# Kernel tuning notes

Hardware: AMD Instinct MI355X
Metric: run time of the kernel (lower is better)

## Reference

```python
import jax, jax.numpy as jnp
import numpy as np

B, T, HID = 2, 2048, 4096
H, KV, D = 32, 4, 128
GROUP = H // KV
SCALE = D ** -0.5
EPS = 1e-6
ROPE_BASE = 10000.0


def rope(x, dims=D, base=ROPE_BASE):
    # mlx-style non-traditional RoPE (rotate halves). x: [B, h, T, D]
    t = x.shape[2]
    inv_freq = base ** (-jnp.arange(0, dims, 2, dtype=jnp.float32) / dims)  # [D/2]
    theta = jnp.arange(t, dtype=jnp.float32)[:, None] * inv_freq[None, :]   # [T, D/2]
    cos, sin = jnp.cos(theta), jnp.sin(theta)
    x1, x2 = x[..., : dims // 2], x[..., dims // 2 :]
    return jnp.concatenate([x1 * cos - x2 * sin, x1 * sin + x2 * cos], axis=-1).astype(x.dtype)


def setup_inputs() -> dict:
    key = jax.random.key(0)
    k1, k2, k3 = jax.random.split(key, 3)
    hidden_states = jax.random.normal(k1, (B, T, HID), dtype=jnp.float32)
    Wqkv = jax.random.normal(k2, ((H + 2 * KV) * D, HID), dtype=jnp.float32) * 0.02
    Wo = jax.random.normal(k3, (HID, H * D), dtype=jnp.float32) * 0.02
    q_weight = jnp.ones((H, D), dtype=jnp.float32)
    k_weight = jnp.ones((KV, D), dtype=jnp.float32)
    return {"hidden_states": hidden_states, "Wqkv": Wqkv, "Wo": Wo,
            "q_weight": q_weight, "k_weight": k_weight}


def reference(hidden_states, Wqkv, Wo, q_weight, k_weight):
    x = hidden_states
    qkv = jnp.einsum('btc,oc->bto', x, Wqkv)
    q, k, v = jnp.split(qkv, [H * D, H * D + KV * D], axis=-1)
    q = q.reshape(B, T, H, D).transpose(0, 2, 1, 3)    # [B,H,T,D]
    k = k.reshape(B, T, KV, D).transpose(0, 2, 1, 3)   # [B,KV,T,D]
    v = v.reshape(B, T, KV, D).transpose(0, 2, 1, 3)
    # Faithful to source: q/k are REPLACED by rsqrt(mean(q^2)) * weight (no q multiply)
    q = jax.lax.rsqrt(jnp.mean(q * q, axis=-1, keepdims=True) + EPS) * q_weight[:, None, :]
    k = jax.lax.rsqrt(jnp.mean(k * k, axis=-1, keepdims=True) + EPS) * k_weight[:, None, :]
    q = rope(q)
    k = rope(k)
    # GQA: repeat kv heads
    k = jnp.repeat(k, GROUP, axis=1)  # [B,H,T,D]
    v = jnp.repeat(v, GROUP, axis=1)
    scores = jnp.einsum('bhqd,bhkd->bhqk', q, k) * SCALE
    attn = jax.nn.softmax(scores, axis=-1)
    out = jnp.einsum('bhqk,bhkd->bhqd', attn, v)
    out = out.transpose(0, 2, 1, 3).reshape(B, T, H * D)
    return jnp.einsum('bto,co->btc', out, Wo)
```

## Files before the change

### kernel.cpp

```cpp
#include <hip/hip_runtime.h>

typedef __bf16 bf16_t;
typedef __bf16 bf16x4 __attribute__((ext_vector_type(4)));
typedef __bf16 bf16x8 __attribute__((ext_vector_type(8)));
typedef float floatx4 __attribute__((ext_vector_type(4)));

__device__ __forceinline__ float bf2f(bf16_t x) { return (float)x; }
__device__ __forceinline__ bf16_t f2bf(float x) { return (bf16_t)x; }

__device__ __forceinline__ void async_copy16(const bf16_t* g, bf16_t* l) {
    __builtin_amdgcn_global_load_lds(
        (const __attribute__((address_space(1))) unsigned int*)g,
        (__attribute__((address_space(3))) unsigned int*)l, 16, 0, 0);
}

__global__ __launch_bounds__(256) void cvt_f32_bf16(const float* __restrict__ in,
                                                    bf16_t* __restrict__ out,
                                                    int n8) {
    int i = blockIdx.x * blockDim.x + threadIdx.x;
    if (i >= n8) return;
    const float4* p = (const float4*)in + (size_t)i * 2;
    float4 a = p[0], b = p[1];
    bf16x8 v;
    v[0] = f2bf(a.x); v[1] = f2bf(a.y); v[2] = f2bf(a.z); v[3] = f2bf(a.w);
    v[4] = f2bf(b.x); v[5] = f2bf(b.y); v[6] = f2bf(b.z); v[7] = f2bf(b.w);
    *(bf16x8*)(out + (size_t)i * 8) = v;
}

template <typename OT>
__global__ __launch_bounds__(256) void gemm_bt(const bf16_t* __restrict__ A,
                                               const bf16_t* __restrict__ B,
                                               OT* __restrict__ C,
                                               int M, int N, int K) {
    __shared__ __attribute__((aligned(16))) bf16_t As[128 * 32];
    __shared__ __attribute__((aligned(16))) bf16_t Bs[128 * 32];
    const int tid = threadIdx.x;
    const int lane = tid & 63;
    const int w = tid >> 6;
    const int l15 = lane & 15, qd = lane >> 4;
    const int tm = blockIdx.y * 128, tn = blockIdx.x * 128;
    const int wm = (w >> 1) * 64, wn = (w & 1) * 64;

    floatx4 acc[4][4] = {};

    for (int k0 = 0; k0 < K; k0 += 32) {
#pragma unroll
        for (int it = 0; it < 2; ++it) {
            int c = it * 256 + tid;
            int row = c >> 2, col = (c & 3) * 8;
            async_copy16(&A[(size_t)(tm + row) * K + k0 + col], &As[c * 8]);
            async_copy16(&B[(size_t)(tn + row) * K + k0 + col], &Bs[c * 8]);
        }
        __syncthreads();
        bf16x8 af[4], bfr[4];
#pragma unroll
        for (int i = 0; i < 4; i++)
            af[i] = *(const bf16x8*)&As[(wm + i * 16 + l15) * 32 + qd * 8];
#pragma unroll
        for (int j = 0; j < 4; j++)
            bfr[j] = *(const bf16x8*)&Bs[(wn + j * 16 + l15) * 32 + qd * 8];
#pragma unroll
        for (int i = 0; i < 4; i++)
#pragma unroll
            for (int j = 0; j < 4; j++)
                acc[i][j] = __builtin_amdgcn_mfma_f32_16x16x32_bf16(
                    af[i], bfr[j], acc[i][j], 0, 0, 0);
        __syncthreads();
    }
#pragma unroll
    for (int i = 0; i < 4; i++) {
        int row = tm + wm + i * 16 + qd * 4;
#pragma unroll
        for (int j = 0; j < 4; j++) {
            int col = tn + wn + j * 16 + l15;
#pragma unroll
            for (int r = 0; r < 4; r++)
                C[(size_t)(row + r) * N + col] = (OT)acc[i][j][r];
        }
    }
}

__global__ __launch_bounds__(256) void rmsrope(const bf16_t* __restrict__ qkv,
                                               const float* __restrict__ qw,
                                               const float* __restrict__ kw,
                                               bf16_t* __restrict__ q_r,
                                               bf16_t* __restrict__ k_r,
                                               bf16_t* __restrict__ v_r) {
    const int tid = threadIdx.x, lane = tid & 63, w = tid >> 6;
    const int slot = blockIdx.x * 4 + w;
    const int row = slot / 40;
    const int hs = slot - row * 40;
    const int b = row >> 11, t = row & 2047;
    const bf16_t* src = qkv + (size_t)row * 5120 + hs * 128;

    if (hs >= 36) {
        size_t dst = ((size_t)((b * 4 + (hs - 36)) * 2048 + t)) * 128;
        v_r[dst + lane] = src[lane];
        v_r[dst + lane + 64] = src[lane + 64];
        return;
    }
    float x1 = bf2f(src[lane]);
    float x2 = bf2f(src[lane + 64]);
    float ss = x1 * x1 + x2 * x2;
#pragma unroll
    for (int off = 1; off < 64; off <<= 1) ss += __shfl_xor(ss, off);
    const float rr = rsqrtf(ss * (1.0f / 128.0f) + 1e-6f);

    const float* wp;
    bf16_t* dstp;
    float sc;
    if (hs < 32) {
        wp = qw + hs * 128;
        dstp = q_r + ((size_t)((b * 32 + hs) * 2048 + t)) * 128;
        sc = rr * (0.08838834764831845f * 1.4426950408889634f);
    } else {
        wp = kw + (hs - 32) * 128;
        dstp = k_r + ((size_t)((b * 4 + (hs - 32)) * 2048 + t)) * 128;
        sc = rr;
    }
    float n1 = sc * wp[lane];
    float n2 = sc * wp[lane + 64];
    float inv_freq = exp2f((float)lane * -0.20762050593046f);
    float th = (float)t * inv_freq;
    float sn, cs;
    sincosf(th, &sn, &cs);
    dstp[lane] = f2bf(n1 * cs - n2 * sn);
    dstp[lane + 64] = f2bf(n1 * sn + n2 * cs);
}

__global__ __launch_bounds__(256, 2) void flash_attn(const bf16_t* __restrict__ Qr,
                                                     const bf16_t* __restrict__ Kr,
                                                     const bf16_t* __restrict__ Vr,
                                                     bf16_t* __restrict__ Oo) {
    __shared__ __attribute__((aligned(16))) bf16_t Ks[64 * 128];
    __shared__ __attribute__((aligned(16))) bf16_t Vts[128 * 72];
    __shared__ __attribute__((aligned(16))) bf16_t Ps[4][32 * 72];
    const int tid = threadIdx.x, lane = tid & 63, w = tid >> 6;
    const int l15 = lane & 15, qd = lane >> 4;
    const int qt = blockIdx.x, bh = blockIdx.y;
    const int b = bh >> 5, h = bh & 31;
    const int kvh = h >> 3;
    const bf16_t* Qb = Qr + ((size_t)(b * 32 + h) * 2048 + qt * 128) * 128;
    const bf16_t* Kb = Kr + ((size_t)(b * 4 + kvh) * 2048) * 128;
    const bf16_t* Vb = Vr + ((size_t)(b * 4 + kvh) * 2048) * 128;
    const int wrow = w * 32;
    const int pi = l15 * 4 + qd;

    bf16x8 qf[2][4];
#pragma unroll
    for (int i = 0; i < 2; i++)
#pragma unroll
        for (int kk = 0; kk < 4; kk++)
            qf[i][kk] = *(const bf16x8*)&Qb[(size_t)(wrow + i * 16 + l15) * 128 +
                                            kk * 32 + qd * 8];

    bf16x8 onef;
#pragma unroll
    for (int e = 0; e < 8; ++e) onef[e] = f2bf(1.0f);

    float m_s[2][4];
    floatx4 lacc[2] = {};
    floatx4 oacc[2][8] = {};
#pragma unroll
    for (int i = 0; i < 2; i++)
#pragma unroll
        for (int r = 0; r < 4; r++) m_s[i][r] = -1e30f;

    for (int kt = 0; kt < 32; ++kt) {
        __syncthreads();
#pragma unroll
        for (int it = 0; it < 4; ++it) {
            int cc = it * 256 + tid;
            int row = cc >> 4;
            int xb = ((cc & 15) * 16) ^ ((row & 7) << 4);
            async_copy16(&Kb[(size_t)(kt * 64 + row) * 128 + (xb >> 1)],
                         &Ks[cc * 8]);
        }
#pragma unroll
        for (int it = 0; it < 4; ++it) {
            int d0 = (it * 4 + w) * 8;
            bf16x8 v = *(const bf16x8*)&Vb[(size_t)(kt * 64 + lane) * 128 + d0];
#pragma unroll
            for (int e = 0; e < 8; ++e) Vts[(d0 + e) * 72 + pi] = v[e];
        }
        __syncthreads();

        floatx4 sacc[2][4] = {};
#pragma unroll
        for (int kk = 0; kk < 4; kk++) {
            bf16x8 bfr[4];
#pragma unroll
            for (int j = 0; j < 4; j++) {
                int rr2 = j * 16 + l15;
                int xb = (kk * 64 + qd * 16) ^ ((rr2 & 7) << 4);
                bfr[j] = *(const bf16x8*)&Ks[rr2 * 128 + (xb >> 1)];
            }
#pragma unroll
            for (int i = 0; i < 2; i++)
#pragma unroll
                for (int j = 0; j < 4; j++)
                    sacc[i][j] = __builtin_amdgcn_mfma_f32_16x16x32_bf16(
                        qf[i][kk], bfr[j], sacc[i][j], 0, 0, 0);
        }

        float mxv[2][4];
        int fneed = 0;
#pragma unroll
        for (int i = 0; i < 2; i++)
#pragma unroll
            for (int r = 0; r < 4; r++) {
                float mx = fmaxf(fmaxf(sacc[i][0][r], sacc[i][1][r]),
                                 fmaxf(sacc[i][2][r], sacc[i][3][r]));
#pragma unroll
                for (int off = 1; off < 16; off <<= 1)
                    mx = fmaxf(mx, __shfl_xor(mx, off));
                mxv[i][r] = mx;
                fneed |= (mx > m_s[i][r] + 11.5f);
            }
        if (__any(fneed)) {
#pragma unroll
            for (int i = 0; i < 2; i++)
#pragma unroll
                for (int r = 0; r < 4; r++) {
                    float mnew = fmaxf(m_s[i][r], mxv[i][r]);
                    float alpha = exp2f(m_s[i][r] - mnew);
                    m_s[i][r] = mnew;
#pragma unroll
                    for (int jo = 0; jo < 8; jo++) oacc[i][jo][r] *= alpha;
                    lacc[i][r] *= alpha;
                }
        }
#pragma unroll
        for (int i = 0; i < 2; i++)
#pragma unroll
            for (int r = 0; r < 4; r++) {
                float m = m_s[i][r];
                bf16x4 pv;
                pv[0] = f2bf(exp2f(sacc[i][0][r] - m));
                pv[1] = f2bf(exp2f(sacc[i][1][r] - m));
                pv[2] = f2bf(exp2f(sacc[i][2][r] - m));
                pv[3] = f2bf(exp2f(sacc[i][3][r] - m));
                *(bf16x4*)&Ps[w][(i * 16 + qd * 4 + r) * 72 + l15 * 4] = pv;
            }

#pragma unroll
        for (int kk = 0; kk < 64; kk += 32) {
            bf16x8 pf[2], vf[8];
#pragma unroll
            for (int i = 0; i < 2; i++)
                pf[i] = *(const bf16x8*)&Ps[w][(i * 16 + l15) * 72 + kk + qd * 8];
#pragma unroll
            for (int jo = 0; jo < 8; jo++)
                vf[jo] = *(const bf16x8*)&Vts[(jo * 16 + l15) * 72 + kk + qd * 8];
#pragma unroll
            for (int i = 0; i < 2; i++) {
                lacc[i] = __builtin_amdgcn_mfma_f32_16x16x32_bf16(
                    pf[i], onef, lacc[i], 0, 0, 0);
#pragma unroll
                for (int jo = 0; jo < 8; jo++)
                    oacc[i][jo] = __builtin_amdgcn_mfma_f32_16x16x32_bf16(
                        pf[i], vf[jo], oacc[i][jo], 0, 0, 0);
            }
        }
    }

#pragma unroll
    for (int i = 0; i < 2; i++) {
#pragma unroll
        for (int r = 0; r < 4; r++) {
            float inv = 1.0f / lacc[i][r];
            int tg = qt * 128 + wrow + i * 16 + qd * 4 + r;
            size_t base = ((size_t)b * 2048 + tg) * 4096 + h * 128;
#pragma unroll
            for (int jo = 0; jo < 8; jo++)
                Oo[base + jo * 16 + l15] = f2bf(oacc[i][jo][r] * inv);
        }
    }
}

extern "C" void kernel_launch(void* const* d_in, const int* in_sizes, int n_in,
                              void* d_out, int out_size, void* d_ws, size_t ws_size,
                              hipStream_t stream) {
    const float* hidden = (const float*)d_in[0];
    const float* Wqkv   = (const float*)d_in[1];
    const float* Wo     = (const float*)d_in[2];
    const float* qw     = (const float*)d_in[3];
    const float* kw     = (const float*)d_in[4];
    float* out = (float*)d_out;

    char* ws = (char*)d_ws;
    bf16_t* Wqkv_bf   = (bf16_t*)ws;
    bf16_t* q_r       = (bf16_t*)ws;
    bf16_t* k_r       = (bf16_t*)(ws + 33554432ull);
    bf16_t* v_r       = (bf16_t*)(ws + 37748736ull);
    bf16_t* hidden_bf = (bf16_t*)(ws + 41943040ull);
    bf16_t* attn      = (bf16_t*)(ws + 41943040ull);
    bf16_t* qkv       = (bf16_t*)(ws + 75497472ull);
    bf16_t* Wo_bf     = (bf16_t*)(ws + 75497472ull);

    hipLaunchKernelGGL(cvt_f32_bf16, dim3(8192), dim3(256), 0, stream,
                       hidden, hidden_bf, 16777216 / 8);
    hipLaunchKernelGGL(cvt_f32_bf16, dim3(10240), dim3(256), 0, stream,
                       Wqkv, Wqkv_bf, 20971520 / 8);
    hipLaunchKernelGGL((gemm_bt<bf16_t>), dim3(40, 32), dim3(256), 0, stream,
                       hidden_bf, Wqkv_bf, qkv, 4096, 5120, 4096);
    hipLaunchKernelGGL(rmsrope, dim3(40960), dim3(256), 0, stream,
                       qkv, qw, kw, q_r, k_r, v_r);
    hipLaunchKernelGGL(cvt_f32_bf16, dim3(8192), dim3(256), 0, stream,
                       Wo, Wo_bf, 16777216 / 8);
    hipLaunchKernelGGL(flash_attn, dim3(16, 64), dim3(256), 0, stream,
                       q_r, k_r, v_r, attn);
    hipLaunchKernelGGL((gemm_bt<float>), dim3(32, 32), dim3(256), 0, stream,
                       attn, Wo_bf, out, 4096, 4096, 4096);
}
```

Baseline: 957.7 us.

## Register-prefetch next K/V tile, use DPP row max, raise attention occupancy

Replaces the async global-to-LDS K copy and the in-loop V load with register prefetch: the next tile's K and V are loaded into registers right after the barrier, so their latency overlaps with the current tile's MFMA and softmax work, and are stored to LDS at the start of the next iteration. The 16-lane max reduction switches from shuffle-xor to DPP row operations, which avoid the LDS-routed permute path. Launch bounds now request 3 blocks per SM. The prefetch adds about 32 VGPRs of live state, and the tighter occupancy target may force spills.

```diff
diff --git a/kernel.cpp b/kernel.cpp
--- a/kernel.cpp
+++ b/kernel.cpp
@@ -12,6 +12,23 @@
     __builtin_amdgcn_global_load_lds(
         (const __attribute__((address_space(1))) unsigned int*)g,
         (__attribute__((address_space(3))) unsigned int*)l, 16, 0, 0);
+}
+
+__device__ __forceinline__ float dpp_max16(float x) {
+    float y;
+    y = __builtin_bit_cast(float, __builtin_amdgcn_mov_dpp(
+            __builtin_bit_cast(int, x), 0xB1, 0xF, 0xF, true));
+    x = fmaxf(x, y);
+    y = __builtin_bit_cast(float, __builtin_amdgcn_mov_dpp(
+            __builtin_bit_cast(int, x), 0x4E, 0xF, 0xF, true));
+    x = fmaxf(x, y);
+    y = __builtin_bit_cast(float, __builtin_amdgcn_mov_dpp(
+            __builtin_bit_cast(int, x), 0x141, 0xF, 0xF, true));
+    x = fmaxf(x, y);
+    y = __builtin_bit_cast(float, __builtin_amdgcn_mov_dpp(
+            __builtin_bit_cast(int, x), 0x140, 0xF, 0xF, true));
+    x = fmaxf(x, y);
+    return x;
 }
 
 __global__ __launch_bounds__(256) void cvt_f32_bf16(const float* __restrict__ in,
@@ -128,7 +145,7 @@
     dstp[lane + 64] = f2bf(n1 * sn + n2 * cs);
 }
 
-__global__ __launch_bounds__(256, 2) void flash_attn(const bf16_t* __restrict__ Qr,
+__global__ __launch_bounds__(256, 3) void flash_attn(const bf16_t* __restrict__ Qr,
                                                      const bf16_t* __restrict__ Kr,
                                                      const bf16_t* __restrict__ Vr,
                                                      bf16_t* __restrict__ Oo) {
@@ -158,6 +175,15 @@
 #pragma unroll
     for (int e = 0; e < 8; ++e) onef[e] = f2bf(1.0f);
 
+    bf16x8 kreg[4], vreg[4];
+#pragma unroll
+    for (int it = 0; it < 4; ++it) {
+        int cc = it * 256 + tid;
+        int row = cc >> 4;
+        kreg[it] = *(const bf16x8*)&Kb[(size_t)row * 128 + (cc & 15) * 8];
+        vreg[it] = *(const bf16x8*)&Vb[(size_t)lane * 128 + (it * 4 + w) * 8];
+    }
+
     float m_s[2][4];
     floatx4 lacc[2] = {};
     floatx4 oacc[2][8] = {};
@@ -173,17 +199,28 @@
             int cc = it * 256 + tid;
             int row = cc >> 4;
             int xb = ((cc & 15) * 16) ^ ((row & 7) << 4);
-            async_copy16(&Kb[(size_t)(kt * 64 + row) * 128 + (xb >> 1)],
-                         &Ks[cc * 8]);
+            *(bf16x8*)&Ks[row * 128 + (xb >> 1)] = kreg[it];
         }
 #pragma unroll
         for (int it = 0; it < 4; ++it) {
             int d0 = (it * 4 + w) * 8;
-            bf16x8 v = *(const bf16x8*)&Vb[(size_t)(kt * 64 + lane) * 128 + d0];
-#pragma unroll
-            for (int e = 0; e < 8; ++e) Vts[(d0 + e) * 72 + pi] = v[e];
+#pragma unroll
+            for (int e = 0; e < 8; ++e) Vts[(d0 + e) * 72 + pi] = vreg[it][e];
         }
         __syncthreads();
+
+        {
+            int ktn = (kt + 1 < 32) ? kt + 1 : kt;
+#pragma unroll
+            for (int it = 0; it < 4; ++it) {
+                int cc = it * 256 + tid;
+                int row = cc >> 4;
+                kreg[it] = *(const bf16x8*)&Kb[(size_t)(ktn * 64 + row) * 128 +
+                                               (cc & 15) * 8];
+                vreg[it] = *(const bf16x8*)&Vb[(size_t)(ktn * 64 + lane) * 128 +
+                                               (it * 4 + w) * 8];
+            }
+        }
 
         floatx4 sacc[2][4] = {};
 #pragma unroll
@@ -211,9 +248,7 @@
             for (int r = 0; r < 4; r++) {
                 float mx = fmaxf(fmaxf(sacc[i][0][r], sacc[i][1][r]),
                                  fmaxf(sacc[i][2][r], sacc[i][3][r]));
-#pragma unroll
-                for (int off = 1; off < 16; off <<= 1)
-                    mx = fmaxf(mx, __shfl_xor(mx, off));
+                mx = dpp_max16(mx);
                 mxv[i][r] = mx;
                 fneed |= (mx > m_s[i][r] + 11.5f);
             }
```

Measured after the change: 952.1 us. Within noise of the previous version (-0.6%).
